# Kernel optimization log

Measured on AMD Instinct MI355X. Metric: run time of the kernel, lower is better.

The kernel has to match this reference:

```python
import jax, jax.numpy as jnp
import numpy as np

R = 2           # local_radius
N_HEADS = 4     # num_heads
OUT = 256       # out_channels


def _attn_scale(x, Wq, bq, Wk, bk, Wv, bv):
    # Faithful jax port of SparseSelfAttention.forward
    B, C, H, W = x.shape
    N = H * W
    d = OUT // N_HEADS
    # torch x.view(B, N, -1) on contiguous [B,C,H,W] == row-major reshape
    xf = x.reshape(B, N, C)
    q = (xf @ Wq.T + bq).reshape(B, N, N_HEADS, d).transpose(0, 2, 1, 3)  # [B,h,N,d]
    k = (xf @ Wk.T + bk).reshape(B, N, N_HEADS, d).transpose(0, 2, 1, 3)
    v = (xf @ Wv.T + bv).reshape(B, N, N_HEADS, d).transpose(0, 2, 1, 3)
    scale = 1.0 / np.sqrt(OUT).astype(np.float32)
    acc = jnp.zeros_like(v)
    for dh in range(-R, R + 1):
        for dw in range(-R, R + 1):
            # original rolls dims (-3,-2) of [B,h,N,d] -> (head, point) dims
            rk = jnp.roll(k, (dh, dw), axis=(1, 2))
            s = jnp.einsum('bhnd,bhmd->bhnm', q, rk) * scale  # [B,h,N,N]
            a = jax.nn.softmax(s, axis=-1)                     # dropout p=0.0
            rv = jnp.roll(v, (-dh, -dw), axis=(1, 2))
            acc = acc + jnp.einsum('bhnm,bhmd->bhnd', a, rv)
    return acc.transpose(0, 2, 1, 3).reshape(B, N, OUT)  # [B,N,out]


def setup_inputs() -> dict:
    key = jax.random.key(0)
    ks = jax.random.split(key, 8)
    B, C, H, W = 2, 256, 32, 32
    std = 1.0 / np.sqrt(C)
    d = {
        'x0': jax.random.normal(ks[0], (B, C, H, W), jnp.float32),
        'x1': jax.random.normal(ks[1], (B, C, H, W), jnp.float32),
    }
    i = 2
    for s in (0, 1):
        for p in ('q', 'k', 'v'):
            d[f'W{p}{s}'] = jax.random.uniform(ks[i], (OUT, C), jnp.float32, -std, std)
            d[f'b{p}{s}'] = jnp.zeros((OUT,), jnp.float32)
            i += 1
    return d


def reference(x0, x1, Wq0, bq0, Wk0, bk0, Wv0, bv0,
              Wq1, bq1, Wk1, bk1, Wv1, bv1):
    out0 = _attn_scale(x0, Wq0, bq0, Wk0, bk0, Wv0, bv0)
    out1 = _attn_scale(x1, Wq1, bq1, Wk1, bk1, Wv1, bv1)
    return out0 + out1  # [B, N, out_channels], summed across scales
```

## Files before the change

### kernel.cpp

```cpp
#include <hip/hip_runtime.h>
#include <hip/hip_bf16.h>


typedef __bf16 bf16x8 __attribute__((ext_vector_type(8)));
typedef __bf16 bf16x4 __attribute__((ext_vector_type(4)));
typedef float f32x4 __attribute__((ext_vector_type(4)));

#define MFMA16(A,B,C) __builtin_amdgcn_mfma_f32_16x16x32_bf16(A,B,C,0,0,0)

__device__ __forceinline__ bf16x8 ld8(const __bf16* p){ return *reinterpret_cast<const bf16x8*>(p); }

struct ProjArgs { const float* W[6]; const float* Bz[6]; };

__global__ __launch_bounds__(256) void cvt_k(const float* __restrict__ x0,
                                             const float* __restrict__ x1,
                                             ProjArgs args,
                                             __bf16* __restrict__ Xb,
                                             __bf16* __restrict__ Wb)
{
    int g = blockIdx.x*256 + threadIdx.x;
    const float* src; __bf16* dst;
    if (g < 131072){
        int s = g >> 16;
        int E = (g & 65535)*8;
        int blk = E >> 9, lane8 = (E >> 3) & 63;
        int row = (blk>>3)*16 + (lane8 & 15);
        int ci  = (blk&7)*32 + (lane8>>4)*8;
        src = (s ? x1 : x0) + (size_t)row*256 + ci;
        dst = Xb + (size_t)s*524288 + E;
    } else {
        int gw = g - 131072;
        int sp = gw >> 13;
        int E = (gw & 8191)*8;
        int blk = E >> 9, lane8 = (E >> 3) & 63;
        int co = (blk>>3)*16 + (lane8 & 15);
        int ci = (blk&7)*32 + (lane8>>4)*8;
        src = args.W[sp] + (size_t)co*256 + ci;
        dst = Wb + (size_t)sp*65536 + E;
    }
    f32x4 a = *reinterpret_cast<const f32x4*>(src);
    f32x4 b = *reinterpret_cast<const f32x4*>(src+4);
    bf16x8 o;
    #pragma unroll
    for (int j=0;j<4;j++){ o[j] = (__bf16)a[j]; o[4+j] = (__bf16)b[j]; }
    *reinterpret_cast<bf16x8*>(dst) = o;
}

__global__ __launch_bounds__(256) void proj_k(const __bf16* __restrict__ Xb,
                                              const __bf16* __restrict__ Wb,
                                              ProjArgs args,
                                              __bf16* __restrict__ Qb,
                                              __bf16* __restrict__ Kb,
                                              __bf16* __restrict__ Vb)
{
    __shared__ __bf16 stage[4096];
    int bid = blockIdx.x;
    int cg = bid % 12, rg = bid / 12;
    int tid = threadIdx.x, wv = tid >> 6, l = tid & 63;
    int lr = l & 15, lg = l >> 4;
    int s = rg >> 5;
    const __bf16* Xf = Xb + (size_t)s*524288;
    int p = cg >> 2;
    const __bf16* Wf = Wb + (size_t)(s*3+p)*65536;
    const float* bp = args.Bz[s*3 + p];
    int colbase = (cg & 3)*64;
    int rowblk = ((rg & 31)*4 + wv);

    f32x4 acc[4];
    #pragma unroll
    for (int t=0;t<4;t++) acc[t] = f32x4{0.f,0.f,0.f,0.f};

    #pragma unroll
    for (int kk=0; kk<8; kk++){
        bf16x8 af = ld8(Xf + (size_t)(rowblk*8 + kk)*512 + l*8);
        #pragma unroll
        for (int ct=0; ct<4; ct++){
            bf16x8 bfv = ld8(Wf + (size_t)(((cg&3)*4 + ct)*8 + kk)*512 + l*8);
            acc[ct] = MFMA16(af, bfv, acc[ct]);
        }
    }
    float qs = (p==0) ? 0.09016844136f : 1.0f;
    #pragma unroll
    for (int ct=0; ct<4; ct++){
        int d = ct*16 + lr;
        float bias = bp[colbase + d];
        #pragma unroll
        for (int i=0;i<4;i++){
            float v = (acc[ct][i] + bias) * qs;
            int a;
            if (p < 2) a = wv*1024 + ((d>>5)&1)*512 + ((d>>3)&3)*128 + (lg*4+i)*8 + (d&7);
            else       a = (wv*16 + lg*4 + i)*64 + d;
            stage[a] = (__bf16)v;
        }
    }
    __syncthreads();
    int gr0 = rg*64;
    int b = (gr0 >> 10) & 1, n0 = gr0 & 1023;
    int h = cg & 3;
    int sb = s*2 + b;
    __bf16* dstb; size_t goff;
    if (p == 0){ dstb = Qb; goff = ((size_t)(sb*4 + h))*65536 + (size_t)(n0>>4)*1024; }
    else if (p == 1){ dstb = Kb; goff = ((size_t)(sb*4 + h))*65536 + (size_t)(n0>>4)*1024; }
    else { dstb = Vb; goff = ((size_t)(sb*4 + h)*1024 + n0)*64; }
    bf16x8 v0 = *reinterpret_cast<const bf16x8*>(stage + tid*16);
    bf16x8 v1 = *reinterpret_cast<const bf16x8*>(stage + tid*16 + 8);
    *reinterpret_cast<bf16x8*>(dstb + goff + (size_t)tid*16)     = v0;
    *reinterpret_cast<bf16x8*>(dstb + goff + (size_t)tid*16 + 8) = v1;
}

__global__ __launch_bounds__(256) void smooth_k(const __bf16* __restrict__ Vb,
                                                __bf16* __restrict__ WT)
{
    __shared__ __bf16 Vt[72][66];
    int bid = blockIdx.x;
    int sbu = bid >> 4, n0 = (bid & 15)*64;
    int tid = threadIdx.x;
    const __bf16* Vs = Vb + (size_t)sbu*65536;
    for (int idx = tid; idx < 576; idx += 256){
        int row = idx >> 3, ch = idx & 7;
        int n = (n0 - 4 + row) & 1023;
        bf16x8 v = ld8(Vs + (size_t)n*64 + ch*8);
        #pragma unroll
        for (int j=0;j<8;j++) Vt[row][ch*8+j] = v[j];
    }
    __syncthreads();
    int w = tid >> 6, l = tid & 63;
    __bf16* dst = WT + (size_t)sbu*65536;
    int m = n0 + l;
    int kb = m >> 5, m32 = m & 31;
    int p = (m32 < 16) ? ((m32>>2)*8 + (m32&3))
                       : (((m32-16)>>2)*8 + 4 + (m32&3));
    size_t pbase = (size_t)kb*2048 + (p>>3)*128 + (p&7);
    #pragma unroll
    for (int it=0; it<16; it++){
        int d = it*4 + w;
        float sum = 0.f;
        #pragma unroll
        for (int j=0;j<5;j++) sum += (float)Vt[l + j*2][d];
        dst[pbase + (size_t)(d>>4)*512 + (d&15)*8] = (__bf16)sum;
    }
}

__global__ __launch_bounds__(256) void attn_k(const __bf16* __restrict__ Qb,
                                              const __bf16* __restrict__ Kb,
                                              const __bf16* __restrict__ WT,
                                              __bf16* __restrict__ pvp)
{
    int tid = threadIdx.x, wv = tid>>6, l = tid&63, lr = l&15, lg = l>>4;
    int t = blockIdx.x;
    int qg = t & 7; t >>= 3;
    int dhi = t & 3, h = (t>>2)&3, b = (t>>4)&1, s = (t>>5)&1;
    int dhv = (dhi==2) ? -1 : (dhi==3 ? 2 : dhi);
    int g = (h - dhv + 4) & 3;
    int u = (h + dhv + 4) & 3;
    int sb = s*2 + b;
    int nbase = qg*128 + wv*32;
    const __bf16* Qw = Qb + ((size_t)(sb*4 + h))*65536 + (size_t)(nbase>>4)*1024;
    const __bf16* Kg = Kb + ((size_t)(sb*4 + g))*65536;
    const __bf16* Wu = WT + ((size_t)(sb*4 + u))*65536;
    bf16x8 qa0 = ld8(Qw + l*8),        qa1 = ld8(Qw + 512 + l*8);
    bf16x8 qb0 = ld8(Qw + 1024 + l*8), qb1 = ld8(Qw + 1536 + l*8);

    const f32x4 z = {0.f,0.f,0.f,0.f};
    f32x4 pvA[4] = {z,z,z,z};
    f32x4 pvB[4] = {z,z,z,z};
    float dsA = 0.f, dsB = 0.f;

    #pragma unroll 2
    for (int kt=0; kt<1024; kt+=32){
        const __bf16* k0 = Kg + (size_t)(kt>>4)*1024 + l*8;
        bf16x8 kf00 = ld8(k0),        kf01 = ld8(k0 + 512);
        bf16x8 kf10 = ld8(k0 + 1024), kf11 = ld8(k0 + 1536);
        const __bf16* w0 = Wu + (size_t)(kt>>5)*2048 + l*8;
        bf16x8 wd0 = ld8(w0);
        bf16x8 wd1 = ld8(w0 + 512);
        bf16x8 wd2 = ld8(w0 + 1024);
        bf16x8 wd3 = ld8(w0 + 1536);
        __builtin_amdgcn_s_setprio(1);
        f32x4 sA0 = MFMA16(kf00, qa0, z); sA0 = MFMA16(kf01, qa1, sA0);
        f32x4 sA1 = MFMA16(kf10, qa0, z); sA1 = MFMA16(kf11, qa1, sA1);
        f32x4 sB0 = MFMA16(kf00, qb0, z); sB0 = MFMA16(kf01, qb1, sB0);
        f32x4 sB1 = MFMA16(kf10, qb0, z); sB1 = MFMA16(kf11, qb1, sB1);
        __builtin_amdgcn_s_setprio(0);
        bf16x8 paA, paB;
        #pragma unroll
        for (int i=0;i<4;i++){
            float eA0 = __builtin_amdgcn_exp2f(sA0[i]);
            float eA1 = __builtin_amdgcn_exp2f(sA1[i]);
            float eB0 = __builtin_amdgcn_exp2f(sB0[i]);
            float eB1 = __builtin_amdgcn_exp2f(sB1[i]);
            dsA += eA0 + eA1;
            dsB += eB0 + eB1;
            paA[i] = (__bf16)eA0; paA[4+i] = (__bf16)eA1;
            paB[i] = (__bf16)eB0; paB[4+i] = (__bf16)eB1;
        }
        __builtin_amdgcn_s_setprio(1);
        pvA[0] = MFMA16(wd0, paA, pvA[0]);
        pvA[1] = MFMA16(wd1, paA, pvA[1]);
        pvA[2] = MFMA16(wd2, paA, pvA[2]);
        pvA[3] = MFMA16(wd3, paA, pvA[3]);
        pvB[0] = MFMA16(wd0, paB, pvB[0]);
        pvB[1] = MFMA16(wd1, paB, pvB[1]);
        pvB[2] = MFMA16(wd2, paB, pvB[2]);
        pvB[3] = MFMA16(wd3, paB, pvB[3]);
        __builtin_amdgcn_s_setprio(0);
    }
    dsA += __shfl_xor(dsA, 16, 64); dsA += __shfl_xor(dsA, 32, 64);
    dsB += __shfl_xor(dsB, 16, 64); dsB += __shfl_xor(dsB, 32, 64);
    float wgt = (dhi==3) ? 2.f : 1.f;
    float invA = wgt / dsA, invB = wgt / dsB;

    __shared__ alignas(16) __bf16 ost[4][32*72];
    __bf16* S = ost[wv];
    #pragma unroll
    for (int dt=0; dt<4; dt++){
        bf16x4 oA, oB;
        #pragma unroll
        for (int i=0;i<4;i++){ oA[i] = (__bf16)(pvA[dt][i]*invA); oB[i] = (__bf16)(pvB[dt][i]*invB); }
        int c0 = dt*16 + lg*4;
        *reinterpret_cast<bf16x4*>(S + lr*72 + c0)      = oA;
        *reinterpret_cast<bf16x4*>(S + (16+lr)*72 + c0) = oB;
    }
    int slot = s*4 + dhi;
    __bf16* pp = pvp + (size_t)slot*524288 + (size_t)b*262144 + (size_t)h*64;
    #pragma unroll
    for (int it=0; it<4; it++){
        int r = it*8 + (l>>3);
        bf16x8 v = *reinterpret_cast<const bf16x8*>(S + r*72 + (l&7)*8);
        *reinterpret_cast<bf16x8*>(pp + (size_t)(nbase + r)*256 + (l&7)*8) = v;
    }
}

__global__ __launch_bounds__(256) void reduce_k(const __bf16* __restrict__ pvp,
                                                float* __restrict__ out)
{
    int idx = blockIdx.x*256 + threadIdx.x;
    size_t off = (size_t)idx*8;
    float acc[8] = {0,0,0,0,0,0,0,0};
    #pragma unroll
    for (int s4=0; s4<8; s4++){
        bf16x8 v = ld8(pvp + (size_t)s4*524288 + off);
        #pragma unroll
        for (int j=0;j<8;j++) acc[j] += (float)v[j];
    }
    f32x4 o0 = {acc[0],acc[1],acc[2],acc[3]};
    f32x4 o1 = {acc[4],acc[5],acc[6],acc[7]};
    *reinterpret_cast<f32x4*>(out + off)     = o0;
    *reinterpret_cast<f32x4*>(out + off + 4) = o1;
}

extern "C" void kernel_launch(void* const* d_in, const int* in_sizes, int n_in,
                              void* d_out, int out_size, void* d_ws, size_t ws_size,
                              hipStream_t stream)
{
    const float* x0 = (const float*)d_in[0];
    const float* x1 = (const float*)d_in[1];
    ProjArgs pa;
    for (int s=0;s<2;s++) for (int p=0;p<3;p++){
        pa.W[s*3+p]  = (const float*)d_in[2 + s*6 + p*2];
        pa.Bz[s*3+p] = (const float*)d_in[3 + s*6 + p*2];
    }
    char* wsb = (char*)d_ws;
    __bf16* Qb = (__bf16*)(wsb);
    __bf16* Kb = (__bf16*)(wsb + (2u<<20));
    __bf16* Vb = (__bf16*)(wsb + (4u<<20));
    __bf16* WT = (__bf16*)(wsb + (6u<<20));
    __bf16* Xb = (__bf16*)(wsb + (8u<<20));
    __bf16* Wb = (__bf16*)(wsb + (10u<<20));
    __bf16* pvp = (__bf16*)(wsb + (11u<<20));

    cvt_k<<<704, 256, 0, stream>>>(x0, x1, pa, Xb, Wb);
    proj_k<<<768, 256, 0, stream>>>(Xb, Wb, pa, Qb, Kb, Vb);
    smooth_k<<<256, 256, 0, stream>>>(Vb, WT);
    attn_k<<<512, 256, 0, stream>>>(Qb, Kb, WT, pvp);
    reduce_k<<<256, 256, 0, stream>>>(pvp, (float*)d_out);
}
```

Baseline: 47.88 us.

## Replace partial-buffer reduction kernel with fp32 atomicAdd into output

Drops the bf16 partial-sum buffer and the separate reduce kernel. Each attention block now accumulates its normalized result directly into the fp32 output with atomicAdd, and the smoothing kernel zeroes the output beforehand. This removes one kernel launch and a round trip through the partial buffer, but adds contention from eight contributors per output element. Summation order also becomes nondeterministic.

Measured after the change: 55.37 us. +15.6%, slower.

```diff
diff --git a/kernel.cpp b/kernel.cpp
--- a/kernel.cpp
+++ b/kernel.cpp
@@ -109,12 +109,19 @@
 }
 
 __global__ __launch_bounds__(256) void smooth_k(const __bf16* __restrict__ Vb,
-                                                __bf16* __restrict__ WT)
+                                                __bf16* __restrict__ WT,
+                                                float* __restrict__ outz)
 {
     __shared__ __bf16 Vt[72][66];
     int bid = blockIdx.x;
     int sbu = bid >> 4, n0 = (bid & 15)*64;
     int tid = threadIdx.x;
+    {
+        f32x4 zz = {0.f,0.f,0.f,0.f};
+        float* oz = outz + (size_t)bid*2048;
+        *reinterpret_cast<f32x4*>(oz + tid*4)        = zz;
+        *reinterpret_cast<f32x4*>(oz + 1024 + tid*4) = zz;
+    }
     const __bf16* Vs = Vb + (size_t)sbu*65536;
     for (int idx = tid; idx < 576; idx += 256){
         int row = idx >> 3, ch = idx & 7;
@@ -144,7 +151,7 @@
 __global__ __launch_bounds__(256) void attn_k(const __bf16* __restrict__ Qb,
                                               const __bf16* __restrict__ Kb,
                                               const __bf16* __restrict__ WT,
-                                              __bf16* __restrict__ pvp)
+                                              float* __restrict__ out)
 {
     int tid = threadIdx.x, wv = tid>>6, l = tid&63, lr = l&15, lg = l>>4;
     int t = blockIdx.x;
@@ -210,43 +217,22 @@
     float wgt = (dhi==3) ? 2.f : 1.f;
     float invA = wgt / dsA, invB = wgt / dsB;
 
-    __shared__ alignas(16) __bf16 ost[4][32*72];
-    __bf16* S = ost[wv];
+    __shared__ alignas(16) float ost[4][32*72];
+    float* S = ost[wv];
     #pragma unroll
     for (int dt=0; dt<4; dt++){
-        bf16x4 oA, oB;
-        #pragma unroll
-        for (int i=0;i<4;i++){ oA[i] = (__bf16)(pvA[dt][i]*invA); oB[i] = (__bf16)(pvB[dt][i]*invB); }
+        f32x4 oA, oB;
+        #pragma unroll
+        for (int i=0;i<4;i++){ oA[i] = pvA[dt][i]*invA; oB[i] = pvB[dt][i]*invB; }
         int c0 = dt*16 + lg*4;
-        *reinterpret_cast<bf16x4*>(S + lr*72 + c0)      = oA;
-        *reinterpret_cast<bf16x4*>(S + (16+lr)*72 + c0) = oB;
-    }
-    int slot = s*4 + dhi;
-    __bf16* pp = pvp + (size_t)slot*524288 + (size_t)b*262144 + (size_t)h*64;
-    #pragma unroll
-    for (int it=0; it<4; it++){
-        int r = it*8 + (l>>3);
-        bf16x8 v = *reinterpret_cast<const bf16x8*>(S + r*72 + (l&7)*8);
-        *reinterpret_cast<bf16x8*>(pp + (size_t)(nbase + r)*256 + (l&7)*8) = v;
-    }
-}
-
-__global__ __launch_bounds__(256) void reduce_k(const __bf16* __restrict__ pvp,
-                                                float* __restrict__ out)
-{
-    int idx = blockIdx.x*256 + threadIdx.x;
-    size_t off = (size_t)idx*8;
-    float acc[8] = {0,0,0,0,0,0,0,0};
-    #pragma unroll
-    for (int s4=0; s4<8; s4++){
-        bf16x8 v = ld8(pvp + (size_t)s4*524288 + off);
-        #pragma unroll
-        for (int j=0;j<8;j++) acc[j] += (float)v[j];
-    }
-    f32x4 o0 = {acc[0],acc[1],acc[2],acc[3]};
-    f32x4 o1 = {acc[4],acc[5],acc[6],acc[7]};
-    *reinterpret_cast<f32x4*>(out + off)     = o0;
-    *reinterpret_cast<f32x4*>(out + off + 4) = o1;
+        *reinterpret_cast<f32x4*>(S + lr*72 + c0)      = oA;
+        *reinterpret_cast<f32x4*>(S + (16+lr)*72 + c0) = oB;
+    }
+    float* orow = out + ((size_t)b*1024 + nbase)*256 + (size_t)h*64 + l;
+    #pragma unroll
+    for (int r=0; r<32; r++){
+        atomicAdd(orow + (size_t)r*256, S[r*72 + l]);
+    }
 }
 
 extern "C" void kernel_launch(void* const* d_in, const int* in_sizes, int n_in,
@@ -267,11 +253,10 @@
     __bf16* WT = (__bf16*)(wsb + (6u<<20));
     __bf16* Xb = (__bf16*)(wsb + (8u<<20));
     __bf16* Wb = (__bf16*)(wsb + (10u<<20));
-    __bf16* pvp = (__bf16*)(wsb + (11u<<20));
+    float*  out = (float*)d_out;
 
     cvt_k<<<704, 256, 0, stream>>>(x0, x1, pa, Xb, Wb);
     proj_k<<<768, 256, 0, stream>>>(Xb, Wb, pa, Qb, Kb, Vb);
-    smooth_k<<<256, 256, 0, stream>>>(Vb, WT);
-    attn_k<<<512, 256, 0, stream>>>(Qb, Kb, WT, pvp);
-    reduce_k<<<256, 256, 0, stream>>>(pvp, (float*)d_out);
-}
+    smooth_k<<<256, 256, 0, stream>>>(Vb, WT, out);
+    attn_k<<<512, 256, 0, stream>>>(Qb, Kb, WT, out);
+}
```

## Switch attention QK and PV matmuls to FP8 with exp-minus-one offset correction

Applied to the files above, without the earlier changes.

Q, K and the smoothed V tensor are now stored as FP8 and the attention kernel uses FP8 MFMA for both the score and PV products, halving operand bytes and using the higher-rate FP8 path. The scale is split evenly between Q and K. To keep precision, the softmax weights are stored as exp(s)-1 in FP8 and a new small kernel computes per-head column sums of V, which are added back before normalisation. This adds a launch and a serial-looped reduction kernel, and risks accuracy loss from FP8 quantisation of scores and values.

Measured after the change: 56.11 us. 17.2% more time.

```diff
diff --git a/kernel.cpp b/kernel.cpp
--- a/kernel.cpp
+++ b/kernel.cpp
@@ -5,10 +5,16 @@
 typedef __bf16 bf16x8 __attribute__((ext_vector_type(8)));
 typedef __bf16 bf16x4 __attribute__((ext_vector_type(4)));
 typedef float f32x4 __attribute__((ext_vector_type(4)));
+typedef long i64;
 
 #define MFMA16(A,B,C) __builtin_amdgcn_mfma_f32_16x16x32_bf16(A,B,C,0,0,0)
+#define MFMA8(A,B,C)  __builtin_amdgcn_mfma_f32_16x16x32_fp8_fp8(A,B,C,0,0,0)
 
 __device__ __forceinline__ bf16x8 ld8(const __bf16* p){ return *reinterpret_cast<const bf16x8*>(p); }
+__device__ __forceinline__ i64 ldl(const unsigned char* p){ return *reinterpret_cast<const i64*>(p); }
+__device__ __forceinline__ unsigned char tofp8(float v){
+    return (unsigned char)(__builtin_amdgcn_cvt_pk_fp8_f32(v, v, 0, false) & 0xff);
+}
 
 struct ProjArgs { const float* W[6]; const float* Bz[6]; };
 
@@ -49,11 +55,11 @@
 __global__ __launch_bounds__(256) void proj_k(const __bf16* __restrict__ Xb,
                                               const __bf16* __restrict__ Wb,
                                               ProjArgs args,
-                                              __bf16* __restrict__ Qb,
-                                              __bf16* __restrict__ Kb,
+                                              unsigned char* __restrict__ Qb,
+                                              unsigned char* __restrict__ Kb,
                                               __bf16* __restrict__ Vb)
 {
-    __shared__ __bf16 stage[4096];
+    __shared__ alignas(16) unsigned char stage[8192];
     int bid = blockIdx.x;
     int cg = bid % 12, rg = bid / 12;
     int tid = threadIdx.x, wv = tid >> 6, l = tid & 63;
@@ -79,7 +85,7 @@
             acc[ct] = MFMA16(af, bfv, acc[ct]);
         }
     }
-    float qs = (p==0) ? 0.09016844136f : 1.0f;
+    float qs = (p < 2) ? 0.30028057f : 1.0f;
     #pragma unroll
     for (int ct=0; ct<4; ct++){
         int d = ct*16 + lr;
@@ -87,10 +93,13 @@
         #pragma unroll
         for (int i=0;i<4;i++){
             float v = (acc[ct][i] + bias) * qs;
-            int a;
-            if (p < 2) a = wv*1024 + ((d>>5)&1)*512 + ((d>>3)&3)*128 + (lg*4+i)*8 + (d&7);
-            else       a = (wv*16 + lg*4 + i)*64 + d;
-            stage[a] = (__bf16)v;
+            if (p < 2){
+                int a = wv*1024 + ((d>>5)&1)*512 + ((d>>3)&3)*128 + (lg*4+i)*8 + (d&7);
+                stage[a] = tofp8(v);
+            } else {
+                __bf16* sh = reinterpret_cast<__bf16*>(stage);
+                sh[(wv*16 + lg*4 + i)*64 + d] = (__bf16)v;
+            }
         }
     }
     __syncthreads();
@@ -98,18 +107,39 @@
     int b = (gr0 >> 10) & 1, n0 = gr0 & 1023;
     int h = cg & 3;
     int sb = s*2 + b;
-    __bf16* dstb; size_t goff;
-    if (p == 0){ dstb = Qb; goff = ((size_t)(sb*4 + h))*65536 + (size_t)(n0>>4)*1024; }
-    else if (p == 1){ dstb = Kb; goff = ((size_t)(sb*4 + h))*65536 + (size_t)(n0>>4)*1024; }
-    else { dstb = Vb; goff = ((size_t)(sb*4 + h)*1024 + n0)*64; }
-    bf16x8 v0 = *reinterpret_cast<const bf16x8*>(stage + tid*16);
-    bf16x8 v1 = *reinterpret_cast<const bf16x8*>(stage + tid*16 + 8);
-    *reinterpret_cast<bf16x8*>(dstb + goff + (size_t)tid*16)     = v0;
-    *reinterpret_cast<bf16x8*>(dstb + goff + (size_t)tid*16 + 8) = v1;
+    if (p < 2){
+        unsigned char* dstb = (p==0) ? Qb : Kb;
+        size_t goff = ((size_t)(sb*4 + h))*65536 + (size_t)(n0>>4)*1024;
+        uint4 v = *reinterpret_cast<const uint4*>(stage + tid*16);
+        *reinterpret_cast<uint4*>(dstb + goff + (size_t)tid*16) = v;
+    } else {
+        size_t goff = ((size_t)(sb*4 + h)*1024 + n0)*64;
+        const __bf16* sh = reinterpret_cast<const __bf16*>(stage);
+        bf16x8 v0 = *reinterpret_cast<const bf16x8*>(sh + tid*16);
+        bf16x8 v1 = *reinterpret_cast<const bf16x8*>(sh + tid*16 + 8);
+        *reinterpret_cast<bf16x8*>(Vb + goff + (size_t)tid*16)     = v0;
+        *reinterpret_cast<bf16x8*>(Vb + goff + (size_t)tid*16 + 8) = v1;
+    }
+}
+
+__global__ __launch_bounds__(256) void vtot_k(const __bf16* __restrict__ Vb,
+                                              float* __restrict__ Wtot)
+{
+    __shared__ float red[4][64];
+    int sbu = blockIdx.x, tid = threadIdx.x;
+    int d = tid & 63, seg = tid >> 6;
+    const __bf16* Vs = Vb + (size_t)sbu*65536;
+    float sum = 0.f;
+    for (int n = seg*256; n < seg*256 + 256; ++n)
+        sum += (float)Vs[(size_t)n*64 + d];
+    red[seg][d] = sum;
+    __syncthreads();
+    if (seg == 0)
+        Wtot[(size_t)sbu*64 + d] = 5.f*(red[0][d]+red[1][d]+red[2][d]+red[3][d]);
 }
 
 __global__ __launch_bounds__(256) void smooth_k(const __bf16* __restrict__ Vb,
-                                                __bf16* __restrict__ WT)
+                                                unsigned char* __restrict__ WT)
 {
     __shared__ __bf16 Vt[72][66];
     int bid = blockIdx.x;
@@ -125,7 +155,7 @@
     }
     __syncthreads();
     int w = tid >> 6, l = tid & 63;
-    __bf16* dst = WT + (size_t)sbu*65536;
+    unsigned char* dst = WT + (size_t)sbu*65536;
     int m = n0 + l;
     int kb = m >> 5, m32 = m & 31;
     int p = (m32 < 16) ? ((m32>>2)*8 + (m32&3))
@@ -137,13 +167,14 @@
         float sum = 0.f;
         #pragma unroll
         for (int j=0;j<5;j++) sum += (float)Vt[l + j*2][d];
-        dst[pbase + (size_t)(d>>4)*512 + (d&15)*8] = (__bf16)sum;
-    }
-}
-
-__global__ __launch_bounds__(256) void attn_k(const __bf16* __restrict__ Qb,
-                                              const __bf16* __restrict__ Kb,
-                                              const __bf16* __restrict__ WT,
+        dst[pbase + (size_t)(d>>4)*512 + (d&15)*8] = tofp8(sum);
+    }
+}
+
+__global__ __launch_bounds__(256) void attn_k(const unsigned char* __restrict__ Qb,
+                                              const unsigned char* __restrict__ Kb,
+                                              const unsigned char* __restrict__ WT,
+                                              const float* __restrict__ Wtot,
                                               __bf16* __restrict__ pvp)
 {
     int tid = threadIdx.x, wv = tid>>6, l = tid&63, lr = l&15, lg = l>>4;
@@ -155,11 +186,11 @@
     int u = (h + dhv + 4) & 3;
     int sb = s*2 + b;
     int nbase = qg*128 + wv*32;
-    const __bf16* Qw = Qb + ((size_t)(sb*4 + h))*65536 + (size_t)(nbase>>4)*1024;
-    const __bf16* Kg = Kb + ((size_t)(sb*4 + g))*65536;
-    const __bf16* Wu = WT + ((size_t)(sb*4 + u))*65536;
-    bf16x8 qa0 = ld8(Qw + l*8),        qa1 = ld8(Qw + 512 + l*8);
-    bf16x8 qb0 = ld8(Qw + 1024 + l*8), qb1 = ld8(Qw + 1536 + l*8);
+    const unsigned char* Qw = Qb + ((size_t)(sb*4 + h))*65536 + (size_t)(nbase>>4)*1024;
+    const unsigned char* Kg = Kb + ((size_t)(sb*4 + g))*65536;
+    const unsigned char* Wu = WT + ((size_t)(sb*4 + u))*65536;
+    i64 qa0 = ldl(Qw + l*8),        qa1 = ldl(Qw + 512 + l*8);
+    i64 qb0 = ldl(Qw + 1024 + l*8), qb1 = ldl(Qw + 1536 + l*8);
 
     const f32x4 z = {0.f,0.f,0.f,0.f};
     f32x4 pvA[4] = {z,z,z,z};
@@ -168,41 +199,58 @@
 
     #pragma unroll 2
     for (int kt=0; kt<1024; kt+=32){
-        const __bf16* k0 = Kg + (size_t)(kt>>4)*1024 + l*8;
-        bf16x8 kf00 = ld8(k0),        kf01 = ld8(k0 + 512);
-        bf16x8 kf10 = ld8(k0 + 1024), kf11 = ld8(k0 + 1536);
-        const __bf16* w0 = Wu + (size_t)(kt>>5)*2048 + l*8;
-        bf16x8 wd0 = ld8(w0);
-        bf16x8 wd1 = ld8(w0 + 512);
-        bf16x8 wd2 = ld8(w0 + 1024);
-        bf16x8 wd3 = ld8(w0 + 1536);
+        const unsigned char* k0 = Kg + (size_t)(kt>>4)*1024 + l*8;
+        i64 kf00 = ldl(k0),        kf01 = ldl(k0 + 512);
+        i64 kf10 = ldl(k0 + 1024), kf11 = ldl(k0 + 1536);
+        const unsigned char* w0 = Wu + (size_t)(kt>>5)*2048 + l*8;
+        i64 wd0 = ldl(w0);
+        i64 wd1 = ldl(w0 + 512);
+        i64 wd2 = ldl(w0 + 1024);
+        i64 wd3 = ldl(w0 + 1536);
         __builtin_amdgcn_s_setprio(1);
-        f32x4 sA0 = MFMA16(kf00, qa0, z); sA0 = MFMA16(kf01, qa1, sA0);
-        f32x4 sA1 = MFMA16(kf10, qa0, z); sA1 = MFMA16(kf11, qa1, sA1);
-        f32x4 sB0 = MFMA16(kf00, qb0, z); sB0 = MFMA16(kf01, qb1, sB0);
-        f32x4 sB1 = MFMA16(kf10, qb0, z); sB1 = MFMA16(kf11, qb1, sB1);
+        f32x4 sA0 = MFMA8(kf00, qa0, z); sA0 = MFMA8(kf01, qa1, sA0);
+        f32x4 sA1 = MFMA8(kf10, qa0, z); sA1 = MFMA8(kf11, qa1, sA1);
+        f32x4 sB0 = MFMA8(kf00, qb0, z); sB0 = MFMA8(kf01, qb1, sB0);
+        f32x4 sB1 = MFMA8(kf10, qb0, z); sB1 = MFMA8(kf11, qb1, sB1);
         __builtin_amdgcn_s_setprio(0);
-        bf16x8 paA, paB;
-        #pragma unroll
-        for (int i=0;i<4;i++){
-            float eA0 = __builtin_amdgcn_exp2f(sA0[i]);
-            float eA1 = __builtin_amdgcn_exp2f(sA1[i]);
-            float eB0 = __builtin_amdgcn_exp2f(sB0[i]);
-            float eB1 = __builtin_amdgcn_exp2f(sB1[i]);
-            dsA += eA0 + eA1;
-            dsB += eB0 + eB1;
-            paA[i] = (__bf16)eA0; paA[4+i] = (__bf16)eA1;
-            paB[i] = (__bf16)eB0; paB[4+i] = (__bf16)eB1;
-        }
+        unsigned aLo=0, aHi=0, bLo=0, bHi=0;
+        float eA0_0 = __builtin_amdgcn_exp2f(sA0[0]);
+        float eA0_1 = __builtin_amdgcn_exp2f(sA0[1]);
+        float eA0_2 = __builtin_amdgcn_exp2f(sA0[2]);
+        float eA0_3 = __builtin_amdgcn_exp2f(sA0[3]);
+        float eA1_0 = __builtin_amdgcn_exp2f(sA1[0]);
+        float eA1_1 = __builtin_amdgcn_exp2f(sA1[1]);
+        float eA1_2 = __builtin_amdgcn_exp2f(sA1[2]);
+        float eA1_3 = __builtin_amdgcn_exp2f(sA1[3]);
+        float eB0_0 = __builtin_amdgcn_exp2f(sB0[0]);
+        float eB0_1 = __builtin_amdgcn_exp2f(sB0[1]);
+        float eB0_2 = __builtin_amdgcn_exp2f(sB0[2]);
+        float eB0_3 = __builtin_amdgcn_exp2f(sB0[3]);
+        float eB1_0 = __builtin_amdgcn_exp2f(sB1[0]);
+        float eB1_1 = __builtin_amdgcn_exp2f(sB1[1]);
+        float eB1_2 = __builtin_amdgcn_exp2f(sB1[2]);
+        float eB1_3 = __builtin_amdgcn_exp2f(sB1[3]);
+        dsA += (eA0_0+eA0_1)+(eA0_2+eA0_3)+(eA1_0+eA1_1)+(eA1_2+eA1_3);
+        dsB += (eB0_0+eB0_1)+(eB0_2+eB0_3)+(eB1_0+eB1_1)+(eB1_2+eB1_3);
+        aLo = __builtin_amdgcn_cvt_pk_fp8_f32(eA0_0-1.f, eA0_1-1.f, aLo, false);
+        aLo = __builtin_amdgcn_cvt_pk_fp8_f32(eA0_2-1.f, eA0_3-1.f, aLo, true);
+        aHi = __builtin_amdgcn_cvt_pk_fp8_f32(eA1_0-1.f, eA1_1-1.f, aHi, false);
+        aHi = __builtin_amdgcn_cvt_pk_fp8_f32(eA1_2-1.f, eA1_3-1.f, aHi, true);
+        bLo = __builtin_amdgcn_cvt_pk_fp8_f32(eB0_0-1.f, eB0_1-1.f, bLo, false);
+        bLo = __builtin_amdgcn_cvt_pk_fp8_f32(eB0_2-1.f, eB0_3-1.f, bLo, true);
+        bHi = __builtin_amdgcn_cvt_pk_fp8_f32(eB1_0-1.f, eB1_1-1.f, bHi, false);
+        bHi = __builtin_amdgcn_cvt_pk_fp8_f32(eB1_2-1.f, eB1_3-1.f, bHi, true);
+        i64 paA = (i64)(((unsigned long long)aHi << 32) | aLo);
+        i64 paB = (i64)(((unsigned long long)bHi << 32) | bLo);
         __builtin_amdgcn_s_setprio(1);
-        pvA[0] = MFMA16(wd0, paA, pvA[0]);
-        pvA[1] = MFMA16(wd1, paA, pvA[1]);
-        pvA[2] = MFMA16(wd2, paA, pvA[2]);
-        pvA[3] = MFMA16(wd3, paA, pvA[3]);
-        pvB[0] = MFMA16(wd0, paB, pvB[0]);
-        pvB[1] = MFMA16(wd1, paB, pvB[1]);
-        pvB[2] = MFMA16(wd2, paB, pvB[2]);
-        pvB[3] = MFMA16(wd3, paB, pvB[3]);
+        pvA[0] = MFMA8(wd0, paA, pvA[0]);
+        pvA[1] = MFMA8(wd1, paA, pvA[1]);
+        pvA[2] = MFMA8(wd2, paA, pvA[2]);
+        pvA[3] = MFMA8(wd3, paA, pvA[3]);
+        pvB[0] = MFMA8(wd0, paB, pvB[0]);
+        pvB[1] = MFMA8(wd1, paB, pvB[1]);
+        pvB[2] = MFMA8(wd2, paB, pvB[2]);
+        pvB[3] = MFMA8(wd3, paB, pvB[3]);
         __builtin_amdgcn_s_setprio(0);
     }
     dsA += __shfl_xor(dsA, 16, 64); dsA += __shfl_xor(dsA, 32, 64);
@@ -210,13 +258,22 @@
     float wgt = (dhi==3) ? 2.f : 1.f;
     float invA = wgt / dsA, invB = wgt / dsB;
 
+    const float* WtU = Wtot + (size_t)(sb*4 + u)*64;
+    f32x4 wt[4];
+    #pragma unroll
+    for (int dt=0; dt<4; dt++)
+        wt[dt] = *reinterpret_cast<const f32x4*>(WtU + dt*16 + lg*4);
+
     __shared__ alignas(16) __bf16 ost[4][32*72];
     __bf16* S = ost[wv];
     #pragma unroll
     for (int dt=0; dt<4; dt++){
         bf16x4 oA, oB;
         #pragma unroll
-        for (int i=0;i<4;i++){ oA[i] = (__bf16)(pvA[dt][i]*invA); oB[i] = (__bf16)(pvB[dt][i]*invB); }
+        for (int i=0;i<4;i++){
+            oA[i] = (__bf16)((pvA[dt][i] + wt[dt][i])*invA);
+            oB[i] = (__bf16)((pvB[dt][i] + wt[dt][i])*invB);
+        }
         int c0 = dt*16 + lg*4;
         *reinterpret_cast<bf16x4*>(S + lr*72 + c0)      = oA;
         *reinterpret_cast<bf16x4*>(S + (16+lr)*72 + c0) = oB;
@@ -261,17 +318,19 @@
         pa.Bz[s*3+p] = (const float*)d_in[3 + s*6 + p*2];
     }
     char* wsb = (char*)d_ws;
-    __bf16* Qb = (__bf16*)(wsb);
-    __bf16* Kb = (__bf16*)(wsb + (2u<<20));
-    __bf16* Vb = (__bf16*)(wsb + (4u<<20));
-    __bf16* WT = (__bf16*)(wsb + (6u<<20));
-    __bf16* Xb = (__bf16*)(wsb + (8u<<20));
-    __bf16* Wb = (__bf16*)(wsb + (10u<<20));
-    __bf16* pvp = (__bf16*)(wsb + (11u<<20));
+    unsigned char* Qb = (unsigned char*)(wsb);
+    unsigned char* Kb = (unsigned char*)(wsb + (1u<<20));
+    __bf16* Vb = (__bf16*)(wsb + (2u<<20));
+    unsigned char* WT = (unsigned char*)(wsb + (4u<<20));
+    __bf16* Xb = (__bf16*)(wsb + (5u<<20));
+    __bf16* Wb = (__bf16*)(wsb + (7u<<20));
+    __bf16* pvp = (__bf16*)(wsb + (8u<<20));
+    float*  Wtot = (float*)(wsb + (16u<<20));
 
     cvt_k<<<704, 256, 0, stream>>>(x0, x1, pa, Xb, Wb);
     proj_k<<<768, 256, 0, stream>>>(Xb, Wb, pa, Qb, Kb, Vb);
+    vtot_k<<<16, 256, 0, stream>>>(Vb, Wtot);
     smooth_k<<<256, 256, 0, stream>>>(Vb, WT);
-    attn_k<<<512, 256, 0, stream>>>(Qb, Kb, WT, pvp);
+    attn_k<<<512, 256, 0, stream>>>(Qb, Kb, WT, Wtot, pvp);
     reduce_k<<<256, 256, 0, stream>>>(pvp, (float*)d_out);
 }
```
